# Kernel optimization log

Measured on AMD Instinct MI355X. Metric: run time of the kernel, lower is better.

## Reference

```python
import jax, jax.numpy as jnp
import numpy as np

NEG_SLOPE = 0.2  # LeakyReLU(0.2)


def setup_inputs() -> dict:
    key = jax.random.key(0)
    k0, k1, kw, kb = jax.random.split(key, 4)
    B, N, M, D, H = 1, 1024, 1024, 256, 128
    z0 = jax.random.normal(k0, (B, N, D), dtype=jnp.float32)
    z1 = jax.random.normal(k1, (B, M, D), dtype=jnp.float32)
    # Conv2d(D, H, 1) weight (H, D, 1, 1) squeezed to (H, D); bias (H,)
    W = jax.random.normal(kw, (H, D), dtype=jnp.float32) * (1.0 / np.sqrt(D))
    bias = jax.random.normal(kb, (H,), dtype=jnp.float32) * 0.01
    return {"z0": z0, "z1": z1, "W": W, "bias": bias}


def reference(z0, z1, W, bias):
    # torch: z_mul[b,d,n,m] = z0[b,n,d] * z1[b,m,d]; c = conv1x1(z_mul); LeakyReLU
    # Fused: 1x1 conv over channel D is a contraction -> single einsum, no (b,D,N,M) intermediate.
    c = jnp.einsum('bnd,bmd,hd->bhnm', z0, z1, W) + bias[None, :, None, None]
    return jnp.where(c >= 0, c, NEG_SLOPE * c)
```

## Files before the change

### kernel.cpp

```cpp
#include <hip/hip_runtime.h>
#include <cstdint>

#define AS1 __attribute__((address_space(1)))
#define AS3 __attribute__((address_space(3)))

typedef __bf16 v8bf __attribute__((ext_vector_type(8)));
typedef float  v4f  __attribute__((ext_vector_type(4)));

__device__ __forceinline__ uint32_t f2u(float f) {
    union { float f; uint32_t u; } v; v.f = f; return v.u;
}
__device__ __forceinline__ uint16_t f2bf_rne(float f) {
    uint32_t u = f2u(f);
    return (uint16_t)((u + 0x7FFFu + ((u >> 16) & 1u)) >> 16);
}
__device__ __forceinline__ uint32_t pack2(float a, float b) {
    return (uint32_t)f2bf_rne(a) | ((uint32_t)f2bf_rne(b) << 16);
}
__device__ __forceinline__ void async16(const void* g, void* l) {
    __builtin_amdgcn_global_load_lds((AS1 const void*)g, (AS3 void*)l, 16, 0, 0);
}

__global__ __launch_bounds__(256)
void prep_kernel(const float* __restrict__ z0, const float* __restrict__ z1,
                 const float* __restrict__ W,
                 uint16_t* __restrict__ Aall, uint16_t* __restrict__ Bbf)
{
    const int b = blockIdx.x;
    if (b < 16384) {
        const size_t e0 = ((size_t)b * 256 + threadIdx.x) * 8;
        const int h  = (int)(e0 >> 18);
        const int nd = (int)(e0 & 0x3FFFFu);
        const int d0 = (int)(e0 & 255u);
        float4 za = *(const float4*)(z0 + nd);
        float4 zb = *(const float4*)(z0 + nd + 4);
        float4 wa = *(const float4*)(W + h * 256 + d0);
        float4 wb = *(const float4*)(W + h * 256 + d0 + 4);
        uint4 r;
        r.x = pack2(za.x * wa.x, za.y * wa.y);
        r.y = pack2(za.z * wa.z, za.w * wa.w);
        r.z = pack2(zb.x * wb.x, zb.y * wb.y);
        r.w = pack2(zb.z * wb.z, zb.w * wb.w);
        *(uint4*)(Aall + e0) = r;
    } else {
        const size_t e0 = ((size_t)(b - 16384) * 256 + threadIdx.x) * 8;
        float4 za = *(const float4*)(z1 + e0);
        float4 zb = *(const float4*)(z1 + e0 + 4);
        uint4 r;
        r.x = pack2(za.x, za.y);
        r.y = pack2(za.z, za.w);
        r.z = pack2(zb.x, zb.y);
        r.w = pack2(zb.z, zb.w);
        *(uint4*)(Bbf + e0) = r;
    }
}

__global__ __launch_bounds__(256)
void gemm_kernel(const uint16_t* __restrict__ Aall, const uint16_t* __restrict__ Bbf,
                 const float* __restrict__ bias, float* __restrict__ out)
{
    __shared__ __align__(16) uint16_t aT[128 * 32];
    __shared__ __align__(16) uint16_t bT[128 * 32];

    const int t = threadIdx.x, wave = t >> 6, lane = t & 63;
    const int h = blockIdx.z, n0 = blockIdx.y * 128, m0 = blockIdx.x * 128;
    const uint16_t* Ab = Aall + ((size_t)h << 18) + ((size_t)n0 << 8);
    const uint16_t* Bb = Bbf + ((size_t)m0 << 8);

    const int rowA = t >> 2;
    const int col8 = (t & 3) * 8;

    v4f acc[4][4];
#pragma unroll
    for (int r = 0; r < 4; ++r)
#pragma unroll
        for (int c = 0; c < 4; ++c) acc[r][c] = (v4f){0.f, 0.f, 0.f, 0.f};

    const int mbw = (wave & 1) * 64;
    const int nb  = (wave >> 1) * 64;
    const int fr  = lane & 15;
    const int kq  = (lane >> 4) * 8;

    for (int ks = 0; ks < 8; ++ks) {
        const int k0 = ks * 32;
        async16(Ab + (size_t)rowA * 256 + k0 + col8,        &aT[(wave * 64) * 8]);
        async16(Ab + (size_t)(rowA + 64) * 256 + k0 + col8, &aT[(256 + wave * 64) * 8]);
        async16(Bb + (size_t)rowA * 256 + k0 + col8,        &bT[(wave * 64) * 8]);
        async16(Bb + (size_t)(rowA + 64) * 256 + k0 + col8, &bT[(256 + wave * 64) * 8]);
        __syncthreads();

        v8bf am[4], bn[4];
#pragma unroll
        for (int r = 0; r < 4; ++r)
            am[r] = *(const v8bf*)&bT[(mbw + r * 16 + fr) * 32 + kq];
#pragma unroll
        for (int c = 0; c < 4; ++c)
            bn[c] = *(const v8bf*)&aT[(nb + c * 16 + fr) * 32 + kq];
#pragma unroll
        for (int r = 0; r < 4; ++r)
#pragma unroll
            for (int c = 0; c < 4; ++c)
                acc[r][c] = __builtin_amdgcn_mfma_f32_16x16x32_bf16(am[r], bn[c], acc[r][c], 0, 0, 0);

        __syncthreads();
    }

    const float bsf = bias[h];
    float* outB = out + ((size_t)h << 20) + ((size_t)n0 << 10) + m0;
    const int mq = (lane >> 4) * 4;
#pragma unroll
    for (int r = 0; r < 4; ++r) {
#pragma unroll
        for (int c = 0; c < 4; ++c) {
            const int n = nb + c * 16 + fr;
            const int m = mbw + r * 16 + mq;
            float4 o;
            float v0 = acc[r][c][0] + bsf; o.x = (v0 >= 0.f) ? v0 : 0.2f * v0;
            float v1 = acc[r][c][1] + bsf; o.y = (v1 >= 0.f) ? v1 : 0.2f * v1;
            float v2 = acc[r][c][2] + bsf; o.z = (v2 >= 0.f) ? v2 : 0.2f * v2;
            float v3 = acc[r][c][3] + bsf; o.w = (v3 >= 0.f) ? v3 : 0.2f * v3;
            *(float4*)(outB + ((size_t)n << 10) + m) = o;
        }
    }
}

__global__ __launch_bounds__(256)
void gemm_fb(const float* __restrict__ z0, const float* __restrict__ z1,
             const float* __restrict__ W, const float* __restrict__ bias,
             float* __restrict__ out)
{
    __shared__ __align__(16) uint16_t aT[128 * 32];
    __shared__ __align__(16) uint16_t bT[128 * 32];
    const int t = threadIdx.x, wave = t >> 6, lane = t & 63;
    const int h = blockIdx.z, n0 = blockIdx.y * 128, m0 = blockIdx.x * 128;
    const float* Ab = z0 + (size_t)n0 * 256;
    const float* Bb = z1 + (size_t)m0 * 256;
    const int rowA = t >> 2, col8 = (t & 3) * 8;

    v4f acc[4][4];
#pragma unroll
    for (int r = 0; r < 4; ++r)
#pragma unroll
        for (int c = 0; c < 4; ++c) acc[r][c] = (v4f){0.f, 0.f, 0.f, 0.f};

    const int mbw = (wave & 1) * 64, nb = (wave >> 1) * 64;
    const int fr = lane & 15, kq = (lane >> 4) * 8;

    for (int ks = 0; ks < 8; ++ks) {
        const int k0 = ks * 32;
        float4 wa = *(const float4*)(W + h * 256 + k0 + col8);
        float4 wb = *(const float4*)(W + h * 256 + k0 + col8 + 4);
#pragma unroll
        for (int i = 0; i < 2; ++i) {
            const int row = i * 64 + rowA;
            float4 za = *(const float4*)(Ab + (size_t)row * 256 + k0 + col8);
            float4 zb = *(const float4*)(Ab + (size_t)row * 256 + k0 + col8 + 4);
            uint4 r;
            r.x = pack2(za.x * wa.x, za.y * wa.y);
            r.y = pack2(za.z * wa.z, za.w * wa.w);
            r.z = pack2(zb.x * wb.x, zb.y * wb.y);
            r.w = pack2(zb.z * wb.z, zb.w * wb.w);
            *(uint4*)&aT[(i * 256 + t) * 8] = r;
            float4 ba = *(const float4*)(Bb + (size_t)row * 256 + k0 + col8);
            float4 bb = *(const float4*)(Bb + (size_t)row * 256 + k0 + col8 + 4);
            uint4 s;
            s.x = pack2(ba.x, ba.y);
            s.y = pack2(ba.z, ba.w);
            s.z = pack2(bb.x, bb.y);
            s.w = pack2(bb.z, bb.w);
            *(uint4*)&bT[(i * 256 + t) * 8] = s;
        }
        __syncthreads();

        v8bf am[4], bn[4];
#pragma unroll
        for (int r = 0; r < 4; ++r)
            am[r] = *(const v8bf*)&bT[(mbw + r * 16 + fr) * 32 + kq];
#pragma unroll
        for (int c = 0; c < 4; ++c)
            bn[c] = *(const v8bf*)&aT[(nb + c * 16 + fr) * 32 + kq];
#pragma unroll
        for (int r = 0; r < 4; ++r)
#pragma unroll
            for (int c = 0; c < 4; ++c)
                acc[r][c] = __builtin_amdgcn_mfma_f32_16x16x32_bf16(am[r], bn[c], acc[r][c], 0, 0, 0);
        __syncthreads();
    }

    const float bsf = bias[h];
    float* outB = out + ((size_t)h << 20) + ((size_t)n0 << 10) + m0;
    const int mq = (lane >> 4) * 4;
#pragma unroll
    for (int r = 0; r < 4; ++r) {
#pragma unroll
        for (int c = 0; c < 4; ++c) {
            const int n = nb + c * 16 + fr;
            const int m = mbw + r * 16 + mq;
            float4 o;
            float v0 = acc[r][c][0] + bsf; o.x = (v0 >= 0.f) ? v0 : 0.2f * v0;
            float v1 = acc[r][c][1] + bsf; o.y = (v1 >= 0.f) ? v1 : 0.2f * v1;
            float v2 = acc[r][c][2] + bsf; o.z = (v2 >= 0.f) ? v2 : 0.2f * v2;
            float v3 = acc[r][c][3] + bsf; o.w = (v3 >= 0.f) ? v3 : 0.2f * v3;
            *(float4*)(outB + ((size_t)n << 10) + m) = o;
        }
    }
}

extern "C" void kernel_launch(void* const* d_in, const int* in_sizes, int n_in,
                              void* d_out, int out_size, void* d_ws, size_t ws_size,
                              hipStream_t stream) {
    (void)in_sizes; (void)n_in; (void)out_size;
    const float* z0   = (const float*)d_in[0];
    const float* z1   = (const float*)d_in[1];
    const float* Wm   = (const float*)d_in[2];
    const float* bias = (const float*)d_in[3];
    float* out = (float*)d_out;

    const size_t aall_bytes = (size_t)128 * 1024 * 256 * 2;
    const size_t need = aall_bytes + (size_t)1024 * 256 * 2;
    dim3 grid(8, 8, 128), block(256);
    if (ws_size >= need) {
        uint16_t* Aall = (uint16_t*)d_ws;
        uint16_t* Bbf  = (uint16_t*)((char*)d_ws + aall_bytes);
        prep_kernel<<<16512, 256, 0, stream>>>(z0, z1, Wm, Aall, Bbf);
        gemm_kernel<<<grid, block, 0, stream>>>(Aall, Bbf, bias, out);
    } else {
        gemm_fb<<<grid, block, 0, stream>>>(z0, z1, Wm, bias, out);
    }
}
```

Before: 648.9 us.

## Double-buffer LDS with 64-wide K tiles, XOR swizzle, and XCD-aware block remap

The GEMM kernel now loads 64-wide K slices into two LDS buffers, prefetching the next slice while MFMAs run on the current one, and halves the number of barrier pairs. LDS rows are XOR-swizzled to avoid bank conflicts on the fragment reads. A 1-D grid is remapped so that consecutive work items land on the same XCD (wg&7 selects a chunk), aiming to improve L2 reuse of A/B tiles. The LDS footprint rises to 64 KB, which may reduce occupancy. The kernel is likely bound by writing the 512 MB output, so gains may be limited.

```diff
diff --git a/kernel.cpp b/kernel.cpp
--- a/kernel.cpp
+++ b/kernel.cpp
@@ -59,16 +59,23 @@
 void gemm_kernel(const uint16_t* __restrict__ Aall, const uint16_t* __restrict__ Bbf,
                  const float* __restrict__ bias, float* __restrict__ out)
 {
-    __shared__ __align__(16) uint16_t aT[128 * 32];
-    __shared__ __align__(16) uint16_t bT[128 * 32];
+    __shared__ __align__(16) uint16_t aT[2][128 * 64];
+    __shared__ __align__(16) uint16_t bT[2][128 * 64];
 
     const int t = threadIdx.x, wave = t >> 6, lane = t & 63;
-    const int h = blockIdx.z, n0 = blockIdx.y * 128, m0 = blockIdx.x * 128;
+
+    const int wg   = blockIdx.x;
+    const int work = ((wg & 7) << 10) | (wg >> 3);
+    const int h    = work >> 6;
+    const int n0   = ((work >> 3) & 7) << 7;
+    const int m0   = (work & 7) << 7;
+
     const uint16_t* Ab = Aall + ((size_t)h << 18) + ((size_t)n0 << 8);
     const uint16_t* Bb = Bbf + ((size_t)m0 << 8);
 
-    const int rowA = t >> 2;
-    const int col8 = (t & 3) * 8;
+    const int srow = lane >> 3;
+    const int slot = lane & 7;
+    const int swz8 = (slot ^ srow) << 3;
 
     v4f acc[4][4];
 #pragma unroll
@@ -79,29 +86,45 @@
     const int mbw = (wave & 1) * 64;
     const int nb  = (wave >> 1) * 64;
     const int fr  = lane & 15;
-    const int kq  = (lane >> 4) * 8;
-
-    for (int ks = 0; ks < 8; ++ks) {
-        const int k0 = ks * 32;
-        async16(Ab + (size_t)rowA * 256 + k0 + col8,        &aT[(wave * 64) * 8]);
-        async16(Ab + (size_t)(rowA + 64) * 256 + k0 + col8, &aT[(256 + wave * 64) * 8]);
-        async16(Bb + (size_t)rowA * 256 + k0 + col8,        &bT[(wave * 64) * 8]);
-        async16(Bb + (size_t)(rowA + 64) * 256 + k0 + col8, &bT[(256 + wave * 64) * 8]);
-        __syncthreads();
-
-        v8bf am[4], bn[4];
-#pragma unroll
-        for (int r = 0; r < 4; ++r)
-            am[r] = *(const v8bf*)&bT[(mbw + r * 16 + fr) * 32 + kq];
-#pragma unroll
-        for (int c = 0; c < 4; ++c)
-            bn[c] = *(const v8bf*)&aT[(nb + c * 16 + fr) * 32 + kq];
-#pragma unroll
-        for (int r = 0; r < 4; ++r)
+    const int q   = lane >> 4;
+    const int sx  = fr & 7;
+
+#pragma unroll
+    for (int j = 0; j < 4; ++j) {
+        const int row = wave * 32 + j * 8;
+        async16(Ab + (size_t)(row + srow) * 256 + swz8, &aT[0][row * 64]);
+        async16(Bb + (size_t)(row + srow) * 256 + swz8, &bT[0][row * 64]);
+    }
+    __syncthreads();
+
+#pragma unroll
+    for (int ks = 0; ks < 4; ++ks) {
+        const int cur = ks & 1, nxt = cur ^ 1;
+        if (ks < 3) {
+            const int kel = (ks + 1) * 64 + swz8;
+#pragma unroll
+            for (int j = 0; j < 4; ++j) {
+                const int row = wave * 32 + j * 8;
+                async16(Ab + (size_t)(row + srow) * 256 + kel, &aT[nxt][row * 64]);
+                async16(Bb + (size_t)(row + srow) * 256 + kel, &bT[nxt][row * 64]);
+            }
+        }
+#pragma unroll
+        for (int ksl = 0; ksl < 2; ++ksl) {
+            const int ko = ((((ksl << 2) | q) ^ sx) << 3);
+            v8bf am[4], bn[4];
+#pragma unroll
+            for (int r = 0; r < 4; ++r)
+                am[r] = *(const v8bf*)&bT[cur][(mbw + r * 16 + fr) * 64 + ko];
 #pragma unroll
             for (int c = 0; c < 4; ++c)
-                acc[r][c] = __builtin_amdgcn_mfma_f32_16x16x32_bf16(am[r], bn[c], acc[r][c], 0, 0, 0);
-
+                bn[c] = *(const v8bf*)&aT[cur][(nb + c * 16 + fr) * 64 + ko];
+#pragma unroll
+            for (int r = 0; r < 4; ++r)
+#pragma unroll
+                for (int c = 0; c < 4; ++c)
+                    acc[r][c] = __builtin_amdgcn_mfma_f32_16x16x32_bf16(am[r], bn[c], acc[r][c], 0, 0, 0);
+        }
         __syncthreads();
     }
 
@@ -218,13 +241,13 @@
 
     const size_t aall_bytes = (size_t)128 * 1024 * 256 * 2;
     const size_t need = aall_bytes + (size_t)1024 * 256 * 2;
-    dim3 grid(8, 8, 128), block(256);
     if (ws_size >= need) {
         uint16_t* Aall = (uint16_t*)d_ws;
         uint16_t* Bbf  = (uint16_t*)((char*)d_ws + aall_bytes);
         prep_kernel<<<16512, 256, 0, stream>>>(z0, z1, Wm, Aall, Bbf);
-        gemm_kernel<<<grid, block, 0, stream>>>(Aall, Bbf, bias, out);
+        gemm_kernel<<<8192, 256, 0, stream>>>(Aall, Bbf, bias, out);
     } else {
+        dim3 grid(8, 8, 128), block(256);
         gemm_fb<<<grid, block, 0, stream>>>(z0, z1, Wm, bias, out);
     }
 }
```

Result: slower. 666.5 us (+2.7%).

## Double-buffer LDS tiles, swizzle LDS layout, and remap workgroups in gemm

Applied to the files above, without the earlier changes.

The gemm kernel now uses two LDS buffers so the async global-to-LDS loads for the next k-step are issued before the MFMAs of the current step. The LDS layout is XOR-swizzled by row to reduce bank conflicts on fragment reads. The launch uses a 1D grid with a remap of workgroups across XCD-interleaved indices, and the k loop is fully unrolled. LDS use doubles, which may reduce occupancy.

```diff
diff --git a/kernel.cpp b/kernel.cpp
--- a/kernel.cpp
+++ b/kernel.cpp
@@ -59,16 +59,24 @@
 void gemm_kernel(const uint16_t* __restrict__ Aall, const uint16_t* __restrict__ Bbf,
                  const float* __restrict__ bias, float* __restrict__ out)
 {
-    __shared__ __align__(16) uint16_t aT[128 * 32];
-    __shared__ __align__(16) uint16_t bT[128 * 32];
+    __shared__ __align__(16) uint16_t aT[2][128 * 32];
+    __shared__ __align__(16) uint16_t bT[2][128 * 32];
 
     const int t = threadIdx.x, wave = t >> 6, lane = t & 63;
-    const int h = blockIdx.z, n0 = blockIdx.y * 128, m0 = blockIdx.x * 128;
+
+    const int wg   = blockIdx.x;
+    const int work = ((wg & 7) << 10) | (wg >> 3);
+    const int h    = work >> 6;
+    const int n0   = ((work >> 3) & 7) << 7;
+    const int m0   = (work & 7) << 7;
+
     const uint16_t* Ab = Aall + ((size_t)h << 18) + ((size_t)n0 << 8);
     const uint16_t* Bb = Bbf + ((size_t)m0 << 8);
 
-    const int rowA = t >> 2;
-    const int col8 = (t & 3) * 8;
+    const int srow  = t >> 2;
+    const int sslot = (t & 3) ^ (srow & 3);
+    const int sgoff = sslot << 3;
+    const int ldsb  = (wave << 9);
 
     v4f acc[4][4];
 #pragma unroll
@@ -79,23 +87,32 @@
     const int mbw = (wave & 1) * 64;
     const int nb  = (wave >> 1) * 64;
     const int fr  = lane & 15;
-    const int kq  = (lane >> 4) * 8;
-
+    const int ko  = (((lane >> 4) ^ (fr & 3)) << 3);
+
+    async16(Ab + (size_t)srow * 256 + sgoff,        &aT[0][ldsb]);
+    async16(Ab + (size_t)(srow + 64) * 256 + sgoff, &aT[0][2048 + ldsb]);
+    async16(Bb + (size_t)srow * 256 + sgoff,        &bT[0][ldsb]);
+    async16(Bb + (size_t)(srow + 64) * 256 + sgoff, &bT[0][2048 + ldsb]);
+    __syncthreads();
+
+#pragma unroll
     for (int ks = 0; ks < 8; ++ks) {
-        const int k0 = ks * 32;
-        async16(Ab + (size_t)rowA * 256 + k0 + col8,        &aT[(wave * 64) * 8]);
-        async16(Ab + (size_t)(rowA + 64) * 256 + k0 + col8, &aT[(256 + wave * 64) * 8]);
-        async16(Bb + (size_t)rowA * 256 + k0 + col8,        &bT[(wave * 64) * 8]);
-        async16(Bb + (size_t)(rowA + 64) * 256 + k0 + col8, &bT[(256 + wave * 64) * 8]);
-        __syncthreads();
+        const int cur = ks & 1, nxt = cur ^ 1;
+        if (ks < 7) {
+            const int kel = (ks + 1) * 32 + sgoff;
+            async16(Ab + (size_t)srow * 256 + kel,        &aT[nxt][ldsb]);
+            async16(Ab + (size_t)(srow + 64) * 256 + kel, &aT[nxt][2048 + ldsb]);
+            async16(Bb + (size_t)srow * 256 + kel,        &bT[nxt][ldsb]);
+            async16(Bb + (size_t)(srow + 64) * 256 + kel, &bT[nxt][2048 + ldsb]);
+        }
 
         v8bf am[4], bn[4];
 #pragma unroll
         for (int r = 0; r < 4; ++r)
-            am[r] = *(const v8bf*)&bT[(mbw + r * 16 + fr) * 32 + kq];
+            am[r] = *(const v8bf*)&bT[cur][(mbw + r * 16 + fr) * 32 + ko];
 #pragma unroll
         for (int c = 0; c < 4; ++c)
-            bn[c] = *(const v8bf*)&aT[(nb + c * 16 + fr) * 32 + kq];
+            bn[c] = *(const v8bf*)&aT[cur][(nb + c * 16 + fr) * 32 + ko];
 #pragma unroll
         for (int r = 0; r < 4; ++r)
 #pragma unroll
@@ -218,13 +235,13 @@
 
     const size_t aall_bytes = (size_t)128 * 1024 * 256 * 2;
     const size_t need = aall_bytes + (size_t)1024 * 256 * 2;
-    dim3 grid(8, 8, 128), block(256);
     if (ws_size >= need) {
         uint16_t* Aall = (uint16_t*)d_ws;
         uint16_t* Bbf  = (uint16_t*)((char*)d_ws + aall_bytes);
         prep_kernel<<<16512, 256, 0, stream>>>(z0, z1, Wm, Aall, Bbf);
-        gemm_kernel<<<grid, block, 0, stream>>>(Aall, Bbf, bias, out);
+        gemm_kernel<<<8192, 256, 0, stream>>>(Aall, Bbf, bias, out);
     } else {
+        dim3 grid(8, 8, 128), block(256);
         gemm_fb<<<grid, block, 0, stream>>>(z0, z1, Wm, bias, out);
     }
 }
```

After: 649.8 us. No clear change (+0.1%).
